# Performance work log

Measured on AMD Instinct MI355X. Metric: run time of the kernel, lower is better.

The kernel has to match this reference:

```python
import jax, jax.numpy as jnp
import numpy as np

# irrep blocks for 0e+1o+2e: dims 1, 3, 5 (total D=9)
BLOCKS = [(0, 1), (1, 4), (4, 9)]

def block_linear(x, W):
    # x: [N, C, 9], W: [3, C, C] -- e3nn Linear mixes channels within each irrep block
    outs = [jnp.einsum('ncd,cq->nqd', x[..., s:e], W[l]) for l, (s, e) in enumerate(BLOCKS)]
    return jnp.concatenate(outs, axis=-1)

def setup_inputs() -> dict:
    key = jax.random.key(0)
    ks = jax.random.split(key, 14)
    N, E, C, D, B, H, Z = 16384, 262144, 32, 9, 8, 64, 4
    inp = {
        'node_feats': jax.random.normal(ks[0], (N, C, D), jnp.float32),
        'node_attrs': jax.random.uniform(ks[1], (N, Z), jnp.float32),
        'edge_feats': jax.random.normal(ks[2], (E, B), jnp.float32),
        'edge_sh': jax.random.normal(ks[3], (E, D), jnp.float32),
        'cutoff': jax.random.uniform(ks[4], (E, 1), jnp.float32),
        # learned params
        'W_up': jax.random.normal(ks[5], (3, C, C), jnp.float32) / np.float32(np.sqrt(C)),
        'W1': jax.random.normal(ks[6], (B, H), jnp.float32) / np.float32(np.sqrt(B)),
        'W2': jax.random.normal(ks[7], (H, H), jnp.float32) / np.float32(np.sqrt(H)),
        'W3': jax.random.normal(ks[8], (H, C), jnp.float32) / np.float32(np.sqrt(H)),
        'W_lin': jax.random.normal(ks[9], (3, C, C), jnp.float32) / np.float32(np.sqrt(C)),
        'W_sc': jax.random.normal(ks[10], (Z, 3, C, C), jnp.float32) / np.float32(np.sqrt(C)),
        # fixed Clebsch-Gordan-like coupling tensor (constant structure of the TP)
        'CG': jax.random.normal(ks[11], (D, D, D), jnp.float32) / np.float32(D),
        'edge_src': jax.random.randint(ks[12], (E,), 0, N, jnp.int32),
        'edge_dst': jax.random.randint(ks[13], (E,), 0, N, jnp.int32),
    }
    return inp

def reference(node_feats, node_attrs, edge_feats, edge_sh, cutoff,
              W_up, W1, W2, W3, W_lin, W_sc, CG, edge_src, edge_dst):
    N = node_feats.shape[0]
    avg_num_neighbors = 16.0
    # linear_up: per-irrep channel mixing
    x = block_linear(node_feats, W_up)
    # radial MLP -> per-edge tensor-product weights, gated by cutoff
    h = jax.nn.silu(edge_feats @ W1)
    h = jax.nn.silu(h @ W2)
    w = (h @ W3) * cutoff  # [E, C]
    # gather source node feats, weighted equivariant tensor product per edge
    xs = x[edge_src]  # [E, C, D]
    m_ij = jnp.einsum('eci,ej,ijk,ec->eck', xs, edge_sh, CG, w)  # [E, C, D]
    # scatter-sum aggregation into destination nodes
    m_i = jax.ops.segment_sum(m_ij, edge_dst, num_segments=N)  # [N, C, D]
    # output linear + neighbor normalization
    m_i = block_linear(m_i, W_lin) / avg_num_neighbors
    # element-dependent self-connection from current message
    W_node = jnp.einsum('nz,zlcq->nlcq', node_attrs, W_sc)  # [N, 3, C, C]
    scs = jnp.concatenate(
        [jnp.einsum('ncd,ncq->nqd', m_i[..., s:e], W_node[:, l]) for l, (s, e) in enumerate(BLOCKS)],
        axis=-1)
    return (m_i, scs)
```

## Files before the change

### kernel.cpp

```cpp
#include <hip/hip_runtime.h>
#include <cstdint>

#define CC 32
#define DD 9
#define CD 288
#define BB 8
#define HH 64
#define ZZ 4
#define NB 8

#if defined(__has_attribute)
#if __has_attribute(amdgpu_waves_per_eu)
#define WPEU44 __attribute__((amdgpu_waves_per_eu(4, 4)))
#else
#define WPEU44
#endif
#else
#define WPEU44
#endif

__device__ __forceinline__ float silu_f(float v) {
  return v / (1.0f + __expf(-v));
}

__device__ __forceinline__ int blk_of(int d) { return d == 0 ? 0 : (d < 4 ? 1 : 2); }

__global__ __launch_bounds__(256) void k_zero(float* __restrict__ p, int n) {
  int i = blockIdx.x * 256 + threadIdx.x;
  if (i < n) p[i] = 0.0f;
}

__global__ __launch_bounds__(256) void k_hist(const int* __restrict__ edst,
                                              int* __restrict__ deg, int E) {
  int e = blockIdx.x * 256 + threadIdx.x;
  if (e < E) atomicAdd(&deg[edst[e]], 1);
}

__global__ __launch_bounds__(1024) void k_scan(const int* __restrict__ deg,
                                               int* __restrict__ offs,
                                               int* __restrict__ cursor, int N) {
  __shared__ int part[1024];
  int t = threadIdx.x;
  int chunk = (N + 1023) >> 10;
  int base = t * chunk;
  int lim = N - base; if (lim > chunk) lim = chunk; if (lim < 0) lim = 0;
  int s = 0;
  for (int i = 0; i < lim; ++i) s += deg[base + i];
  part[t] = s;
  __syncthreads();
  for (int off = 1; off < 1024; off <<= 1) {
    int v = part[t];
    int u = (t >= off) ? part[t - off] : 0;
    __syncthreads();
    part[t] = v + u;
    __syncthreads();
  }
  int run = (t == 0) ? 0 : part[t - 1];
  for (int i = 0; i < lim; ++i) {
    offs[base + i] = run;
    cursor[base + i] = run;
    run += deg[base + i];
  }
  if (t == 1023) offs[N] = run;
}

__global__ __launch_bounds__(256) void k_scatter(const int* __restrict__ edst,
                                                 int* __restrict__ cursor,
                                                 int* __restrict__ eidx, int E) {
  int e = blockIdx.x * 256 + threadIdx.x;
  if (e < E) {
    int d = edst[e];
    int pos = atomicAdd(&cursor[d], 1);
    eidx[pos] = e;
  }
}

__global__ __launch_bounds__(256) void k_w2t(const float* __restrict__ W2,
                                             float* __restrict__ W2T) {
  int t = blockIdx.x * 256 + threadIdx.x;
  int q = t >> 6, k = t & 63;
  W2T[t] = W2[k * HH + q];
}

__global__ __launch_bounds__(288) void k_linear_up(
    const float* __restrict__ nf, const float* __restrict__ Wup,
    float* __restrict__ x, int N) {
  __shared__ float snf[NB][DD * 36];
  int t = threadIdx.x;
  int g = t >> 5, q = t & 31;
  int tc = t / 9, td = t - tc * 9;
  int l0 = blk_of(g);
  float wcol[CC];
#pragma unroll
  for (int c = 0; c < CC; ++c) wcol[c] = Wup[l0 * 1024 + c * 32 + q];
  int n0 = blockIdx.x * NB;
#pragma unroll
  for (int nb = 0; nb < NB; ++nb) {
    if (n0 + nb < N) snf[nb][td * 36 + tc] = nf[(size_t)(n0 + nb) * CD + t];
  }
  __syncthreads();
#pragma unroll
  for (int nb = 0; nb < NB; ++nb) {
    if (n0 + nb >= N) break;
    const float4* rowp = (const float4*)(snf[nb] + g * 36);
    float a0 = 0.f, a1 = 0.f;
#pragma unroll
    for (int c4 = 0; c4 < 8; ++c4) {
      float4 b = rowp[c4];
      a0 += b.x * wcol[c4 * 4 + 0] + b.y * wcol[c4 * 4 + 1];
      a1 += b.z * wcol[c4 * 4 + 2] + b.w * wcol[c4 * 4 + 3];
    }
    x[(size_t)(n0 + nb) * CD + t] = a0 + a1;
  }
}

__global__ __launch_bounds__(256) WPEU44 void k_mlp(
    const float* __restrict__ ef, const float* __restrict__ cut,
    const float* __restrict__ W1, const float* __restrict__ W2T,
    const float* __restrict__ W3, float* __restrict__ w, int E) {
  int e = blockIdx.x * 256 + threadIdx.x;
  if (e >= E) return;
  const float4* efp = (const float4*)(ef + (size_t)e * BB);
  float4 efa = efp[0];
  float4 efb = efp[1];
  float efv[BB] = {efa.x, efa.y, efa.z, efa.w, efb.x, efb.y, efb.z, efb.w};
  float h1[HH];
#pragma unroll
  for (int q = 0; q < HH; ++q) {
    float a = 0.f;
#pragma unroll
    for (int k = 0; k < BB; ++k) a += efv[k] * W1[k * HH + q];
    h1[q] = silu_f(a);
  }
#pragma unroll
  for (int q = 0; q < HH; ++q) asm volatile("" : "+v"(h1[q]));
  float wacc[CC];
#pragma unroll
  for (int c = 0; c < CC; ++c) { wacc[c] = 0.f; asm volatile("" : "+v"(wacc[c])); }
  for (int q = 0; q < HH; ++q) {
    const float* r2 = W2T + q * HH;
    float a0 = 0.f, a1 = 0.f, a2 = 0.f, a3 = 0.f;
#pragma unroll
    for (int k = 0; k < HH; k += 4) {
      a0 += h1[k + 0] * r2[k + 0];
      a1 += h1[k + 1] * r2[k + 1];
      a2 += h1[k + 2] * r2[k + 2];
      a3 += h1[k + 3] * r2[k + 3];
    }
    float h2 = silu_f((a0 + a1) + (a2 + a3));
    const float* r3 = W3 + q * CC;
#pragma unroll
    for (int c = 0; c < CC; ++c) wacc[c] += h2 * r3[c];
  }
  float cv = cut[e];
  float4* wp = (float4*)(w + (size_t)e * CC);
#pragma unroll
  for (int i = 0; i < 8; ++i) {
    float4 v;
    v.x = wacc[i * 4 + 0] * cv;
    v.y = wacc[i * 4 + 1] * cv;
    v.z = wacc[i * 4 + 2] * cv;
    v.w = wacc[i * 4 + 3] * cv;
    wp[i] = v;
  }
}

__global__ __launch_bounds__(256) void k_gather(
    const float* __restrict__ x, const float* __restrict__ w,
    const float* __restrict__ esh, const float* __restrict__ CG,
    const int* __restrict__ offs, const int* __restrict__ eidx,
    const int* __restrict__ esrc, float* __restrict__ mpre, int N) {
  int wid = (blockIdx.x * 256 + threadIdx.x) >> 6;
  if (wid >= N) return;
  int lane = threadIdx.x & 63;
  int h = lane >> 5, c = lane & 31;
  int beg = offs[wid], end = offs[wid + 1];
  float P[81];
#pragma unroll
  for (int i = 0; i < 81; ++i) P[i] = 0.f;
  for (int p0 = beg; p0 < end; p0 += 2) {
    int p = p0 + h;
    bool ok = p < end;
    int pp = ok ? p : p0;
    int e = eidx[pp];
    int s = esrc[e];
    float wc = ok ? w[(size_t)e * CC + c] : 0.f;
    const float* shp = esh + (size_t)e * DD;
    float sh[DD];
#pragma unroll
    for (int j = 0; j < DD; ++j) sh[j] = shp[j];
    const float* xp = x + (size_t)s * CD + c;
    float xs[DD];
#pragma unroll
    for (int i = 0; i < DD; ++i) xs[i] = xp[i * 32];
#pragma unroll
    for (int i = 0; i < DD; ++i) {
      float t = wc * xs[i];
#pragma unroll
      for (int j = 0; j < DD; ++j) P[i * DD + j] += t * sh[j];
    }
  }
  float m[DD];
#pragma unroll
  for (int k = 0; k < DD; ++k) m[k] = 0.f;
#pragma unroll
  for (int i = 0; i < DD; ++i) {
#pragma unroll
    for (int j = 0; j < DD; ++j) {
      float p = P[i * DD + j];
#pragma unroll
      for (int k = 0; k < DD; ++k) m[k] += p * CG[i * 81 + j * DD + k];
    }
  }
#pragma unroll
  for (int k = 0; k < DD; ++k) m[k] += __shfl_xor(m[k], 32);
  if (h == 0) {
    float* mp = mpre + (size_t)wid * CD + c;
#pragma unroll
    for (int k = 0; k < DD; ++k) mp[k * 32] = m[k];
  }
}

__global__ __launch_bounds__(288, 1) void k_out(
    const float* __restrict__ attrs, const float* __restrict__ Wlin,
    const float* __restrict__ Wsc,
    float* __restrict__ out1, float* __restrict__ out2, int N) {
  __shared__ float smp[NB][CD];
  __shared__ float smt[NB][CD];
  __shared__ float sres1[NB * CD];
  __shared__ float sres2[NB * CD];
  int t = threadIdx.x;
  int g = t >> 5, q = t & 31;
  int l0 = blk_of(g);
  float wl[CC];
#pragma unroll
  for (int c = 0; c < CC; ++c) wl[c] = Wlin[l0 * 1024 + c * 32 + q];
  float ws0[CC], ws1[CC], ws2[CC], ws3[CC];
#pragma unroll
  for (int c = 0; c < CC; ++c) {
    ws0[c] = Wsc[0 * 3072 + l0 * 1024 + c * 32 + q];
    ws1[c] = Wsc[1 * 3072 + l0 * 1024 + c * 32 + q];
    ws2[c] = Wsc[2 * 3072 + l0 * 1024 + c * 32 + q];
    ws3[c] = Wsc[3 * 3072 + l0 * 1024 + c * 32 + q];
  }
  int nbat = (N + NB - 1) / NB;
  int b = blockIdx.x;
  float r[NB];
  if (b < nbat) {
#pragma unroll
    for (int nb = 0; nb < NB; ++nb) r[nb] = out2[(size_t)(b * NB + nb) * CD + t];
  }
  for (; b < nbat; b += gridDim.x) {
    int n0 = b * NB;
    __syncthreads();
#pragma unroll
    for (int nb = 0; nb < NB; ++nb) smp[nb][t] = r[nb];
    float4 av[NB];
#pragma unroll
    for (int nb = 0; nb < NB; ++nb) av[nb] = ((const float4*)attrs)[n0 + nb];
    __syncthreads();
    int b2 = b + gridDim.x;
    if (b2 < nbat) {
#pragma unroll
      for (int nb = 0; nb < NB; ++nb) r[nb] = out2[(size_t)(b2 * NB + nb) * CD + t];
    }
#pragma unroll
    for (int nb = 0; nb < NB; ++nb) {
      const float4* rowp = (const float4*)(smp[nb] + g * 32);
      float b0 = 0.f, b1 = 0.f;
#pragma unroll
      for (int c4 = 0; c4 < 8; ++c4) {
        float4 bb = rowp[c4];
        b0 += bb.x * wl[c4 * 4 + 0] + bb.y * wl[c4 * 4 + 1];
        b1 += bb.z * wl[c4 * 4 + 2] + bb.w * wl[c4 * 4 + 3];
      }
      float v = (b0 + b1) * (1.0f / 16.0f);
      smt[nb][t] = v;
      sres1[nb * CD + q * DD + g] = v;
    }
    __syncthreads();
#pragma unroll
    for (int nb = 0; nb < NB; ++nb) {
      const float4* rowp = (const float4*)(smt[nb] + g * 32);
      float z0 = 0.f, z1 = 0.f, z2 = 0.f, z3 = 0.f;
#pragma unroll
      for (int c4 = 0; c4 < 8; ++c4) {
        float4 bb = rowp[c4];
#pragma unroll
        for (int j = 0; j < 4; ++j) {
          float bv = (j == 0) ? bb.x : (j == 1) ? bb.y : (j == 2) ? bb.z : bb.w;
          int c = c4 * 4 + j;
          z0 += bv * ws0[c];
          z1 += bv * ws1[c];
          z2 += bv * ws2[c];
          z3 += bv * ws3[c];
        }
      }
      float4 a = av[nb];
      sres2[nb * CD + q * DD + g] = a.x * z0 + a.y * z1 + a.z * z2 + a.w * z3;
    }
    __syncthreads();
#pragma unroll
    for (int rr = 0; rr < (NB * 72) / 288; ++rr) {
      int s = rr * 288 + t;
      int nb = s / 72, idx = s - nb * 72;
      ((float4*)(out1 + (size_t)(n0 + nb) * CD))[idx] = ((const float4*)sres1)[s];
      ((float4*)(out2 + (size_t)(n0 + nb) * CD))[idx] = ((const float4*)sres2)[s];
    }
  }
}

extern "C" void kernel_launch(void* const* d_in, const int* in_sizes, int n_in,
                              void* d_out, int out_size, void* d_ws, size_t ws_size,
                              hipStream_t stream) {
  const float* nf    = (const float*)d_in[0];
  const float* attrs = (const float*)d_in[1];
  const float* ef    = (const float*)d_in[2];
  const float* esh   = (const float*)d_in[3];
  const float* cutv  = (const float*)d_in[4];
  const float* Wup   = (const float*)d_in[5];
  const float* W1    = (const float*)d_in[6];
  const float* W2    = (const float*)d_in[7];
  const float* W3    = (const float*)d_in[8];
  const float* Wlin  = (const float*)d_in[9];
  const float* Wsc   = (const float*)d_in[10];
  const float* CG    = (const float*)d_in[11];
  const int* esrc    = (const int*)d_in[12];
  const int* edst    = (const int*)d_in[13];
  int N = in_sizes[0] / CD;
  int E = in_sizes[12];
  float* out1 = (float*)d_out;
  float* out2 = out1 + (size_t)N * CD;

  float* x    = (float*)d_ws;
  float* w    = x + (size_t)N * CD;
  int* deg    = (int*)(w + (size_t)E * CC);
  int* offs   = deg + N;
  int* cursor = offs + N + 1;
  int* eidx   = cursor + N;
  float* W2T  = (float*)(eidx + E);

  int nblk = (N + NB - 1) / NB;
  k_zero<<<(N + 255) / 256, 256, 0, stream>>>((float*)deg, N);
  k_hist<<<(E + 255) / 256, 256, 0, stream>>>(edst, deg, E);
  k_scan<<<1, 1024, 0, stream>>>(deg, offs, cursor, N);
  k_scatter<<<(E + 255) / 256, 256, 0, stream>>>(edst, cursor, eidx, E);
  k_w2t<<<16, 256, 0, stream>>>(W2, W2T);
  k_linear_up<<<nblk, 288, 0, stream>>>(nf, Wup, x, N);
  k_mlp<<<(E + 255) / 256, 256, 0, stream>>>(ef, cutv, W1, W2T, W3, w, E);
  k_gather<<<(N + 3) / 4, 256, 0, stream>>>(x, w, esh, CG, offs, eidx, esrc, out2, N);
  k_out<<<512, 288, 0, stream>>>(attrs, Wlin, Wsc, out1, out2, N);
}
```

Before: 269.4 us.

## Store node features as packed bf16 and pre-sort edge data by destination

The up-projected node features are now stored as packed bf16 pairs, which roughly halves the bytes read by each random source gather. The scatter step also records each edge's sorted position. The MLP weights, spherical harmonics and source indices are then written in destination-sorted order, so the gather kernel reads them contiguously instead of through an edge-index indirection. The cost is an extra permutation kernel, scattered writes in the MLP, more workspace, and reduced precision of x in the tensor product, which could break tolerance.

```diff
diff --git a/kernel.cpp b/kernel.cpp
--- a/kernel.cpp
+++ b/kernel.cpp
@@ -24,6 +24,13 @@
 }
 
 __device__ __forceinline__ int blk_of(int d) { return d == 0 ? 0 : (d < 4 ? 1 : 2); }
+
+__device__ __forceinline__ unsigned int f2bf(float f) {
+  unsigned int u = __float_as_uint(f);
+  return (u + 0x7fffu + ((u >> 16) & 1u)) >> 16;
+}
+__device__ __forceinline__ float bf_lo(unsigned int u) { return __uint_as_float(u << 16); }
+__device__ __forceinline__ float bf_hi(unsigned int u) { return __uint_as_float(u & 0xffff0000u); }
 
 __global__ __launch_bounds__(256) void k_zero(float* __restrict__ p, int n) {
   int i = blockIdx.x * 256 + threadIdx.x;
@@ -65,13 +72,29 @@
 }
 
 __global__ __launch_bounds__(256) void k_scatter(const int* __restrict__ edst,
+                                                 const int* __restrict__ esrc,
                                                  int* __restrict__ cursor,
-                                                 int* __restrict__ eidx, int E) {
+                                                 int* __restrict__ eidx,
+                                                 int* __restrict__ srcs,
+                                                 int* __restrict__ rank, int E) {
   int e = blockIdx.x * 256 + threadIdx.x;
   if (e < E) {
     int d = edst[e];
     int pos = atomicAdd(&cursor[d], 1);
     eidx[pos] = e;
+    srcs[pos] = esrc[e];
+    rank[e] = pos;
+  }
+}
+
+__global__ __launch_bounds__(256) void k_eshs(const int* __restrict__ eidx,
+                                              const float* __restrict__ esh,
+                                              float* __restrict__ esh_s, long total) {
+  long i = (long)blockIdx.x * 256 + threadIdx.x;
+  if (i < total) {
+    long pos = i / 9;
+    int j = (int)(i - pos * 9);
+    esh_s[i] = esh[(size_t)eidx[pos] * 9 + j];
   }
 }
 
@@ -84,8 +107,9 @@
 
 __global__ __launch_bounds__(288) void k_linear_up(
     const float* __restrict__ nf, const float* __restrict__ Wup,
-    float* __restrict__ x, int N) {
+    unsigned int* __restrict__ x_p, int N) {
   __shared__ float snf[NB][DD * 36];
+  __shared__ float sval[NB][DD][CC];
   int t = threadIdx.x;
   int g = t >> 5, q = t & 31;
   int tc = t / 9, td = t - tc * 9;
@@ -110,14 +134,29 @@
       a0 += b.x * wcol[c4 * 4 + 0] + b.y * wcol[c4 * 4 + 1];
       a1 += b.z * wcol[c4 * 4 + 2] + b.w * wcol[c4 * 4 + 3];
     }
-    x[(size_t)(n0 + nb) * CD + t] = a0 + a1;
+    sval[nb][g][q] = a0 + a1;
+  }
+  __syncthreads();
+#pragma unroll
+  for (int it = 0; it < 5; ++it) {
+    int idx = it * 288 + t;
+    if (idx < NB * 160) {
+      int nb = idx / 160, r = idx - nb * 160;
+      int p = r >> 5, c = r & 31;
+      if (n0 + nb < N) {
+        unsigned int lo = f2bf(sval[nb][2 * p][c]);
+        unsigned int hi = (p < 4) ? f2bf(sval[nb][2 * p + 1][c]) : 0u;
+        x_p[(size_t)(n0 + nb) * 160 + r] = lo | (hi << 16);
+      }
+    }
   }
 }
 
 __global__ __launch_bounds__(256) WPEU44 void k_mlp(
     const float* __restrict__ ef, const float* __restrict__ cut,
     const float* __restrict__ W1, const float* __restrict__ W2T,
-    const float* __restrict__ W3, float* __restrict__ w, int E) {
+    const float* __restrict__ W3, const int* __restrict__ rank,
+    float* __restrict__ w_s, int E) {
   int e = blockIdx.x * 256 + threadIdx.x;
   if (e >= E) return;
   const float4* efp = (const float4*)(ef + (size_t)e * BB);
@@ -153,7 +192,7 @@
     for (int c = 0; c < CC; ++c) wacc[c] += h2 * r3[c];
   }
   float cv = cut[e];
-  float4* wp = (float4*)(w + (size_t)e * CC);
+  float4* wp = (float4*)(w_s + (size_t)rank[e] * CC);
 #pragma unroll
   for (int i = 0; i < 8; ++i) {
     float4 v;
@@ -166,10 +205,10 @@
 }
 
 __global__ __launch_bounds__(256) void k_gather(
-    const float* __restrict__ x, const float* __restrict__ w,
-    const float* __restrict__ esh, const float* __restrict__ CG,
-    const int* __restrict__ offs, const int* __restrict__ eidx,
-    const int* __restrict__ esrc, float* __restrict__ mpre, int N) {
+    const unsigned int* __restrict__ x_p, const float* __restrict__ w_s,
+    const float* __restrict__ esh_s, const float* __restrict__ CG,
+    const int* __restrict__ offs, const int* __restrict__ srcs,
+    float* __restrict__ mpre, int N) {
   int wid = (blockIdx.x * 256 + threadIdx.x) >> 6;
   if (wid >= N) return;
   int lane = threadIdx.x & 63;
@@ -182,17 +221,20 @@
     int p = p0 + h;
     bool ok = p < end;
     int pp = ok ? p : p0;
-    int e = eidx[pp];
-    int s = esrc[e];
-    float wc = ok ? w[(size_t)e * CC + c] : 0.f;
-    const float* shp = esh + (size_t)e * DD;
+    int s = srcs[pp];
+    float wc = ok ? w_s[(size_t)pp * CC + c] : 0.f;
+    const float* shp = esh_s + (size_t)pp * DD;
     float sh[DD];
 #pragma unroll
     for (int j = 0; j < DD; ++j) sh[j] = shp[j];
-    const float* xp = x + (size_t)s * CD + c;
+    const unsigned int* xp = x_p + (size_t)s * 160 + c;
+    unsigned int u0 = xp[0], u1 = xp[32], u2 = xp[64], u3 = xp[96], u4 = xp[128];
     float xs[DD];
-#pragma unroll
-    for (int i = 0; i < DD; ++i) xs[i] = xp[i * 32];
+    xs[0] = bf_lo(u0); xs[1] = bf_hi(u0);
+    xs[2] = bf_lo(u1); xs[3] = bf_hi(u1);
+    xs[4] = bf_lo(u2); xs[5] = bf_hi(u2);
+    xs[6] = bf_lo(u3); xs[7] = bf_hi(u3);
+    xs[8] = bf_lo(u4);
 #pragma unroll
     for (int i = 0; i < DD; ++i) {
       float t = wc * xs[i];
@@ -332,22 +374,26 @@
   float* out1 = (float*)d_out;
   float* out2 = out1 + (size_t)N * CD;
 
-  float* x    = (float*)d_ws;
-  float* w    = x + (size_t)N * CD;
-  int* deg    = (int*)(w + (size_t)E * CC);
-  int* offs   = deg + N;
-  int* cursor = offs + N + 1;
-  int* eidx   = cursor + N;
-  float* W2T  = (float*)(eidx + E);
+  unsigned int* x_p = (unsigned int*)d_ws;
+  float* w_s   = (float*)(x_p + (size_t)N * 160);
+  float* esh_s = w_s + (size_t)E * CC;
+  int* deg     = (int*)(esh_s + (size_t)E * DD);
+  int* offs    = deg + N;
+  int* cursor  = offs + N + 1;
+  int* eidx    = cursor + N;
+  int* srcs    = eidx + E;
+  int* rank    = srcs + E;
+  float* W2T   = (float*)(rank + E);
 
   int nblk = (N + NB - 1) / NB;
   k_zero<<<(N + 255) / 256, 256, 0, stream>>>((float*)deg, N);
   k_hist<<<(E + 255) / 256, 256, 0, stream>>>(edst, deg, E);
   k_scan<<<1, 1024, 0, stream>>>(deg, offs, cursor, N);
-  k_scatter<<<(E + 255) / 256, 256, 0, stream>>>(edst, cursor, eidx, E);
+  k_scatter<<<(E + 255) / 256, 256, 0, stream>>>(edst, esrc, cursor, eidx, srcs, rank, E);
+  k_eshs<<<(int)(((long)E * 9 + 255) / 256), 256, 0, stream>>>(eidx, esh, esh_s, (long)E * 9);
   k_w2t<<<16, 256, 0, stream>>>(W2, W2T);
-  k_linear_up<<<nblk, 288, 0, stream>>>(nf, Wup, x, N);
-  k_mlp<<<(E + 255) / 256, 256, 0, stream>>>(ef, cutv, W1, W2T, W3, w, E);
-  k_gather<<<(N + 3) / 4, 256, 0, stream>>>(x, w, esh, CG, offs, eidx, esrc, out2, N);
+  k_linear_up<<<nblk, 288, 0, stream>>>(nf, Wup, x_p, N);
+  k_mlp<<<(E + 255) / 256, 256, 0, stream>>>(ef, cutv, W1, W2T, W3, rank, w_s, E);
+  k_gather<<<(N + 3) / 4, 256, 0, stream>>>(x_p, w_s, esh_s, CG, offs, srcs, out2, N);
   k_out<<<512, 288, 0, stream>>>(attrs, Wlin, Wsc, out1, out2, N);
 }
```

New measurement: 263.6 us. 2.2% less time.
